# Kernel tuning notes

Hardware: AMD Instinct MI355X
Metric: run time of the kernel (lower is better)

## Reference

```python
import jax, jax.numpy as jnp
import numpy as np

D_MODEL = 1024


def pos_encoding(seq_len, d_model):
    # pos: [S,1], i: [d/2]
    pos = jnp.arange(seq_len, dtype=jnp.float32)[:, None]
    i = jnp.arange(0, d_model, 2, dtype=jnp.float32)
    angle_rates = 1.0 / jnp.power(10000.0, i / d_model)
    angle_rads = pos * angle_rates  # [S, d/2]
    # NOTE: original concatenates sin block then cos block (not interleaved)
    return jnp.concatenate([jnp.sin(angle_rads), jnp.cos(angle_rads)], axis=-1)  # [S, d]


def setup_inputs() -> dict:
    key = jax.random.key(0)
    ks = jax.random.split(key, 4)
    B, S, D = 4, 2048, D_MODEL
    scale = 1.0 / np.sqrt(D)
    x = jax.random.normal(ks[0], (B, S, D), dtype=jnp.float32)
    Wq = jax.random.normal(ks[1], (D, D), dtype=jnp.float32) * scale
    Wk = jax.random.normal(ks[2], (D, D), dtype=jnp.float32) * scale
    Wv = jax.random.normal(ks[3], (D, D), dtype=jnp.float32) * scale
    bq = jnp.zeros((D,), dtype=jnp.float32)
    bk = jnp.zeros((D,), dtype=jnp.float32)
    bv = jnp.zeros((D,), dtype=jnp.float32)
    return {"x": x, "Wq": Wq, "bq": bq, "Wk": Wk, "bk": bk, "Wv": Wv, "bv": bv}


def reference(x, Wq, bq, Wk, bk, Wv, bv):
    B, S, D = x.shape
    pe = pos_encoding(S, D)  # [S, D]
    h = x + pe[None, :, :]
    q = jnp.einsum('bsd,de->bse', h, Wq) + bq
    k = jnp.einsum('bsd,de->bse', h, Wk) + bk
    v = jnp.einsum('bsd,de->bse', h, Wv) + bv
    logits = jnp.einsum('bqd,bkd->bqk', q, k) / jnp.sqrt(jnp.float32(D))
    attn = jax.nn.softmax(logits, axis=-1)
    out = jnp.einsum('bqk,bkd->bqd', attn, v)
    return x + out
```

## Files before the change

kernel.cpp:

```cpp
#include <hip/hip_runtime.h>
#include <stdint.h>


#define AS1(p) ((__attribute__((address_space(1))) void*)(p))
#define AS3(p) ((__attribute__((address_space(3))) void*)(p))

typedef _Float16 f16x8 __attribute__((ext_vector_type(8)));
typedef _Float16 f16x4 __attribute__((ext_vector_type(4)));
typedef float f32x4 __attribute__((ext_vector_type(4)));

__global__ __launch_bounds__(256) void make_h(const float* __restrict__ x,
                                              _Float16* __restrict__ h) {
  const size_t gid = (size_t)blockIdx.x * 256 + threadIdx.x;
  const size_t e = gid * 4;
  const int d = (int)(e & 1023);
  const int m = (int)(e >> 10);
  const int s = m & 2047;
  const float4 xv = *(const float4*)(x + e);
  const int half = d >> 9;
  const int j0 = d & 511;
  const float c = -0.017988946039016f;
  float p[4];
#pragma unroll
  for (int t = 0; t < 4; t++) {
    const float r = __expf((float)(j0 + t) * c);
    const float a = (float)s * r;
    p[t] = half ? __cosf(a) : __sinf(a);
  }
  f16x4 o;
  o[0] = (_Float16)(xv.x + p[0]);
  o[1] = (_Float16)(xv.y + p[1]);
  o[2] = (_Float16)(xv.z + p[2]);
  o[3] = (_Float16)(xv.w + p[3]);
  *(f16x4*)(h + e) = o;
}

__global__ __launch_bounds__(256) void transpose_w(const float* __restrict__ Wq,
                                                   const float* __restrict__ Wk,
                                                   const float* __restrict__ Wv,
                                                   _Float16* __restrict__ Wt) {
  __shared__ float t[32][33];
  const int z = blockIdx.z;
  const float* W = (z == 0) ? Wq : (z == 1) ? Wk : Wv;
  _Float16* o = Wt + (size_t)z * 1024 * 1024;
  const int tx = threadIdx.x, ty = threadIdx.y;
  const int n0 = blockIdx.x * 32, k0 = blockIdx.y * 32;
#pragma unroll
  for (int i = ty; i < 32; i += 8)
    t[i][tx] = W[(size_t)(k0 + i) * 1024 + (n0 + tx)];
  __syncthreads();
#pragma unroll
  for (int i = ty; i < 32; i += 8)
    o[(size_t)(n0 + i) * 1024 + (k0 + tx)] = (_Float16)t[tx][i];
}

__global__ __launch_bounds__(256) void transpose_v(const _Float16* __restrict__ v,
                                                   _Float16* __restrict__ vT) {
  __shared__ _Float16 t[32][33];
  const int z = blockIdx.z;
  const _Float16* in = v + (size_t)z * 2048 * 1024;
  _Float16* out = vT + (size_t)z * 1024 * 2048;
  const int tx = threadIdx.x, ty = threadIdx.y;
  const int d0 = blockIdx.x * 32, j0 = blockIdx.y * 32;
#pragma unroll
  for (int i = ty; i < 32; i += 8)
    t[i][tx] = in[(size_t)(j0 + i) * 1024 + (d0 + tx)];
  __syncthreads();
#pragma unroll
  for (int i = ty; i < 32; i += 8)
    out[(size_t)(d0 + i) * 2048 + (j0 + tx)] = t[tx][i];
}

__global__ __launch_bounds__(256) void softmax_rows(const _Float16* __restrict__ L,
                                                    _Float16* __restrict__ P) {
  const size_t row = blockIdx.x;
  const _Float16* lr = L + row * 2048;
  _Float16* pr = P + row * 2048;
  const int tid = threadIdx.x;
  const f16x8 v = *(const f16x8*)(lr + tid * 8);
  float f[8];
#pragma unroll
  for (int t = 0; t < 8; t++) f[t] = (float)v[t];
  float mx = f[0];
#pragma unroll
  for (int t = 1; t < 8; t++) mx = fmaxf(mx, f[t]);
#pragma unroll
  for (int off = 32; off > 0; off >>= 1) mx = fmaxf(mx, __shfl_xor(mx, off));
  __shared__ float redm[4];
  __shared__ float reds[4];
  const int lane = tid & 63, wave = tid >> 6;
  if (lane == 0) redm[wave] = mx;
  __syncthreads();
  mx = fmaxf(fmaxf(redm[0], redm[1]), fmaxf(redm[2], redm[3]));
  float e[8];
  float sm = 0.f;
#pragma unroll
  for (int t = 0; t < 8; t++) { e[t] = __expf(f[t] - mx); sm += e[t]; }
#pragma unroll
  for (int off = 32; off > 0; off >>= 1) sm += __shfl_xor(sm, off);
  if (lane == 0) reds[wave] = sm;
  __syncthreads();
  sm = reds[0] + reds[1] + reds[2] + reds[3];
  const float inv = 1.0f / sm;
  f16x8 o;
#pragma unroll
  for (int t = 0; t < 8; t++) o[t] = (_Float16)(e[t] * inv);
  *(f16x8*)(pr + tid * 8) = o;
}

template <int MODE>
__global__ __launch_bounds__(256) void gemm_bt(
    const _Float16* __restrict__ A0, long long sA,
    const _Float16* __restrict__ B0, long long sB,
    void* __restrict__ C0, long long sC,
    const float* __restrict__ aux0, const float* __restrict__ aux1,
    const float* __restrict__ aux2, long long sX,
    const int K, const int N) {
  __shared__ __align__(16) _Float16 As[128 * 32];
  __shared__ __align__(16) _Float16 Bs[128 * 32];
  const int tid = threadIdx.x;
  const int z = blockIdx.z;
  const int bm0 = blockIdx.x * 128, bn0 = blockIdx.y * 128;
  const _Float16* A = A0 + (size_t)z * sA;
  const _Float16* Bt = B0 + (size_t)z * sB;

  const int srow = tid >> 2;
  const int csrc = (tid & 3) ^ ((tid >> 4) & 3);
  const _Float16* a0 = A + (size_t)(bm0 + srow) * K + csrc * 8;
  const _Float16* a1 = a0 + (size_t)64 * K;
  const _Float16* b0 = Bt + (size_t)(bn0 + srow) * K + csrc * 8;
  const _Float16* b1 = b0 + (size_t)64 * K;

  const int lane = tid & 63, wave = tid >> 6;
  const int wr = wave >> 1, wc = wave & 1;
  const int quad = lane >> 4, l16 = lane & 15;
  const int cq = (quad ^ ((l16 >> 2) & 3)) * 8;

  f32x4 acc[4][4];
#pragma unroll
  for (int i = 0; i < 4; i++)
#pragma unroll
    for (int j = 0; j < 4; j++) {
      f32x4 zz = {0.f, 0.f, 0.f, 0.f};
      acc[i][j] = zz;
    }

  for (int k0 = 0; k0 < K; k0 += 32) {
    __syncthreads();
    __builtin_amdgcn_global_load_lds(AS1(a0 + k0), AS3(&As[tid * 8]), 16, 0, 0);
    __builtin_amdgcn_global_load_lds(AS1(a1 + k0), AS3(&As[tid * 8 + 2048]), 16, 0, 0);
    __builtin_amdgcn_global_load_lds(AS1(b0 + k0), AS3(&Bs[tid * 8]), 16, 0, 0);
    __builtin_amdgcn_global_load_lds(AS1(b1 + k0), AS3(&Bs[tid * 8 + 2048]), 16, 0, 0);
    __syncthreads();
    f16x8 af[4], bfr[4];
#pragma unroll
    for (int i = 0; i < 4; i++)
      af[i] = *(const f16x8*)&As[(wr * 64 + i * 16 + l16) * 32 + cq];
#pragma unroll
    for (int j = 0; j < 4; j++)
      bfr[j] = *(const f16x8*)&Bs[(wc * 64 + j * 16 + l16) * 32 + cq];
#pragma unroll
    for (int i = 0; i < 4; i++)
#pragma unroll
      for (int j = 0; j < 4; j++)
        acc[i][j] = __builtin_amdgcn_mfma_f32_16x16x32_f16(af[i], bfr[j],
                                                           acc[i][j], 0, 0, 0);
  }

  const int rowb = bm0 + wr * 64 + quad * 4;
  const int colb = bn0 + wc * 64 + l16;
  if (MODE == 0 || MODE == 1) {
    _Float16* C = (_Float16*)C0 + (size_t)z * sC;
    const float* bias = (z == 0) ? aux0 : (z == 1) ? aux1 : aux2;
#pragma unroll
    for (int i = 0; i < 4; i++)
#pragma unroll
      for (int j = 0; j < 4; j++) {
        const int gn = colb + j * 16;
        const float bb = (MODE == 0) ? bias[gn] : 0.f;
#pragma unroll
        for (int r = 0; r < 4; r++) {
          const float val = (MODE == 0) ? (acc[i][j][r] + bb)
                                        : (acc[i][j][r] * 0.03125f);
          C[(size_t)(rowb + i * 16 + r) * N + gn] = (_Float16)val;
        }
      }
  } else {
    float* C = (float*)C0 + (size_t)z * sC;
    const float* X = aux0 + (size_t)z * sX;
#pragma unroll
    for (int i = 0; i < 4; i++)
#pragma unroll
      for (int j = 0; j < 4; j++)
#pragma unroll
        for (int r = 0; r < 4; r++) {
          const size_t idx = (size_t)(rowb + i * 16 + r) * N + (colb + j * 16);
          C[idx] = acc[i][j][r] + X[idx];
        }
  }
}

extern "C" void kernel_launch(void* const* d_in, const int* in_sizes, int n_in,
                              void* d_out, int out_size, void* d_ws, size_t ws_size,
                              hipStream_t stream) {
  (void)in_sizes; (void)n_in; (void)out_size; (void)ws_size;
  const float* x  = (const float*)d_in[0];
  const float* Wq = (const float*)d_in[1];
  const float* bq = (const float*)d_in[2];
  const float* Wk = (const float*)d_in[3];
  const float* bk = (const float*)d_in[4];
  const float* Wv = (const float*)d_in[5];
  const float* bv = (const float*)d_in[6];
  float* out = (float*)d_out;
  char* ws = (char*)d_ws;

  _Float16* h      = (_Float16*)(ws);
  _Float16* vT     = (_Float16*)(ws);
  _Float16* Wt     = (_Float16*)(ws + 16777216);
  _Float16* qkv    = (_Float16*)(ws + 23068672);
  _Float16* attn   = (_Float16*)(ws + 23068672);
  _Float16* logits = (_Float16*)(ws + 73400320);

  const long long E = 8388608;

  transpose_w<<<dim3(32, 32, 3), dim3(32, 8), 0, stream>>>(Wq, Wk, Wv, Wt);
  make_h<<<8192, 256, 0, stream>>>(x, h);

  gemm_bt<0><<<dim3(64, 8, 3), 256, 0, stream>>>(
      h, 0LL, Wt, 1048576LL, qkv, E, bq, bk, bv, 0LL, 1024, 1024);

  transpose_v<<<dim3(32, 64, 4), dim3(32, 8), 0, stream>>>(qkv + 2 * E, vT);

  gemm_bt<1><<<dim3(16, 16, 4), 256, 0, stream>>>(
      qkv, 2097152LL, qkv + E, 2097152LL, logits, 4194304LL,
      nullptr, nullptr, nullptr, 0LL, 1024, 2048);

  softmax_rows<<<8192, 256, 0, stream>>>(logits, attn);

  gemm_bt<2><<<dim3(16, 8, 4), 256, 0, stream>>>(
      attn, 4194304LL, vT, 2097152LL, out, 2097152LL,
      x, nullptr, nullptr, 2097152LL, 2048, 1024);
}
```

Before: 314.4 us.

## Fuse V transpose into QKV GEMM epilogue and write transposed vectorized outputs

The separate V transpose kernel is removed. The QKV projection now writes V directly in transposed layout from its epilogue. The logits and output GEMMs swap their A/B operand roles so each thread's accumulator column becomes contiguous, which allows 4-wide f16 and float4 stores and loads in the epilogues instead of scattered scalar accesses. This also drops the XOR swizzle on the LDS tile layout, which simplifies address math but risks LDS bank conflicts on the fragment reads.

```diff
diff --git a/kernel.cpp b/kernel.cpp
--- a/kernel.cpp
+++ b/kernel.cpp
@@ -54,23 +54,6 @@
     o[(size_t)(n0 + i) * 1024 + (k0 + tx)] = (_Float16)t[tx][i];
 }
 
-__global__ __launch_bounds__(256) void transpose_v(const _Float16* __restrict__ v,
-                                                   _Float16* __restrict__ vT) {
-  __shared__ _Float16 t[32][33];
-  const int z = blockIdx.z;
-  const _Float16* in = v + (size_t)z * 2048 * 1024;
-  _Float16* out = vT + (size_t)z * 1024 * 2048;
-  const int tx = threadIdx.x, ty = threadIdx.y;
-  const int d0 = blockIdx.x * 32, j0 = blockIdx.y * 32;
-#pragma unroll
-  for (int i = ty; i < 32; i += 8)
-    t[i][tx] = in[(size_t)(j0 + i) * 1024 + (d0 + tx)];
-  __syncthreads();
-#pragma unroll
-  for (int i = ty; i < 32; i += 8)
-    out[(size_t)(d0 + i) * 2048 + (j0 + tx)] = t[tx][i];
-}
-
 __global__ __launch_bounds__(256) void softmax_rows(const _Float16* __restrict__ L,
                                                     _Float16* __restrict__ P) {
   const size_t row = blockIdx.x;
@@ -112,10 +95,10 @@
 __global__ __launch_bounds__(256) void gemm_bt(
     const _Float16* __restrict__ A0, long long sA,
     const _Float16* __restrict__ B0, long long sB,
-    void* __restrict__ C0, long long sC,
+    void* __restrict__ C0, long long sC, void* __restrict__ C1,
     const float* __restrict__ aux0, const float* __restrict__ aux1,
     const float* __restrict__ aux2, long long sX,
-    const int K, const int N) {
+    const int K, const int N, const int ldc) {
   __shared__ __align__(16) _Float16 As[128 * 32];
   __shared__ __align__(16) _Float16 Bs[128 * 32];
   const int tid = threadIdx.x;
@@ -124,17 +107,14 @@
   const _Float16* A = A0 + (size_t)z * sA;
   const _Float16* Bt = B0 + (size_t)z * sB;
 
-  const int srow = tid >> 2;
-  const int csrc = (tid & 3) ^ ((tid >> 4) & 3);
-  const _Float16* a0 = A + (size_t)(bm0 + srow) * K + csrc * 8;
+  const _Float16* a0 = A + (size_t)(bm0 + (tid >> 2)) * K + (tid & 3) * 8;
   const _Float16* a1 = a0 + (size_t)64 * K;
-  const _Float16* b0 = Bt + (size_t)(bn0 + srow) * K + csrc * 8;
+  const _Float16* b0 = Bt + (size_t)(bn0 + (tid >> 2)) * K + (tid & 3) * 8;
   const _Float16* b1 = b0 + (size_t)64 * K;
 
   const int lane = tid & 63, wave = tid >> 6;
   const int wr = wave >> 1, wc = wave & 1;
   const int quad = lane >> 4, l16 = lane & 15;
-  const int cq = (quad ^ ((l16 >> 2) & 3)) * 8;
 
   f32x4 acc[4][4];
 #pragma unroll
@@ -155,10 +135,10 @@
     f16x8 af[4], bfr[4];
 #pragma unroll
     for (int i = 0; i < 4; i++)
-      af[i] = *(const f16x8*)&As[(wr * 64 + i * 16 + l16) * 32 + cq];
+      af[i] = *(const f16x8*)&As[(wr * 64 + i * 16 + l16) * 32 + quad * 8];
 #pragma unroll
     for (int j = 0; j < 4; j++)
-      bfr[j] = *(const f16x8*)&Bs[(wc * 64 + j * 16 + l16) * 32 + cq];
+      bfr[j] = *(const f16x8*)&Bs[(wc * 64 + j * 16 + l16) * 32 + quad * 8];
 #pragma unroll
     for (int i = 0; i < 4; i++)
 #pragma unroll
@@ -169,21 +149,47 @@
 
   const int rowb = bm0 + wr * 64 + quad * 4;
   const int colb = bn0 + wc * 64 + l16;
-  if (MODE == 0 || MODE == 1) {
+  if (MODE == 0) {
+    const float* bias = (z == 0) ? aux0 : (z == 1) ? aux1 : aux2;
+    if (z < 2) {
+      _Float16* C = (_Float16*)C0 + (size_t)z * sC;
+#pragma unroll
+      for (int i = 0; i < 4; i++)
+#pragma unroll
+        for (int j = 0; j < 4; j++) {
+          const int gn = colb + j * 16;
+          const float bb = bias[gn];
+#pragma unroll
+          for (int r = 0; r < 4; r++)
+            C[(size_t)(rowb + i * 16 + r) * N + gn] = (_Float16)(acc[i][j][r] + bb);
+        }
+    } else {
+      _Float16* VT = (_Float16*)C1;
+      const int b = rowb >> 11;
+      const int s0 = (rowb & 2047);
+#pragma unroll
+      for (int i = 0; i < 4; i++)
+#pragma unroll
+        for (int j = 0; j < 4; j++) {
+          const int gn = colb + j * 16;
+          const float bb = bias[gn];
+          f16x4 o;
+#pragma unroll
+          for (int r = 0; r < 4; r++) o[r] = (_Float16)(acc[i][j][r] + bb);
+          *(f16x4*)&VT[(size_t)b * 2097152 + (size_t)gn * 2048 + s0 + i * 16] = o;
+        }
+    }
+  } else if (MODE == 1) {
     _Float16* C = (_Float16*)C0 + (size_t)z * sC;
-    const float* bias = (z == 0) ? aux0 : (z == 1) ? aux1 : aux2;
 #pragma unroll
     for (int i = 0; i < 4; i++)
 #pragma unroll
       for (int j = 0; j < 4; j++) {
         const int gn = colb + j * 16;
-        const float bb = (MODE == 0) ? bias[gn] : 0.f;
-#pragma unroll
-        for (int r = 0; r < 4; r++) {
-          const float val = (MODE == 0) ? (acc[i][j][r] + bb)
-                                        : (acc[i][j][r] * 0.03125f);
-          C[(size_t)(rowb + i * 16 + r) * N + gn] = (_Float16)val;
-        }
+        f16x4 o;
+#pragma unroll
+        for (int r = 0; r < 4; r++) o[r] = (_Float16)(acc[i][j][r] * 0.03125f);
+        *(f16x4*)&C[(size_t)gn * ldc + rowb + i * 16] = o;
       }
   } else {
     float* C = (float*)C0 + (size_t)z * sC;
@@ -191,12 +197,17 @@
 #pragma unroll
     for (int i = 0; i < 4; i++)
 #pragma unroll
-      for (int j = 0; j < 4; j++)
-#pragma unroll
-        for (int r = 0; r < 4; r++) {
-          const size_t idx = (size_t)(rowb + i * 16 + r) * N + (colb + j * 16);
-          C[idx] = acc[i][j][r] + X[idx];
-        }
+      for (int j = 0; j < 4; j++) {
+        const int gn = colb + j * 16;
+        const size_t base = (size_t)gn * ldc + rowb + i * 16;
+        const float4 xv = *(const float4*)(X + base);
+        float4 o;
+        o.x = acc[i][j][0] + xv.x;
+        o.y = acc[i][j][1] + xv.y;
+        o.z = acc[i][j][2] + xv.z;
+        o.w = acc[i][j][3] + xv.w;
+        *(float4*)(C + base) = o;
+      }
   }
 }
 
@@ -215,10 +226,10 @@
   char* ws = (char*)d_ws;
 
   _Float16* h      = (_Float16*)(ws);
-  _Float16* vT     = (_Float16*)(ws);
   _Float16* Wt     = (_Float16*)(ws + 16777216);
-  _Float16* qkv    = (_Float16*)(ws + 23068672);
+  _Float16* qk     = (_Float16*)(ws + 23068672);
   _Float16* attn   = (_Float16*)(ws + 23068672);
+  _Float16* vT     = (_Float16*)(ws + 56623104);
   _Float16* logits = (_Float16*)(ws + 73400320);
 
   const long long E = 8388608;
@@ -227,17 +238,15 @@
   make_h<<<8192, 256, 0, stream>>>(x, h);
 
   gemm_bt<0><<<dim3(64, 8, 3), 256, 0, stream>>>(
-      h, 0LL, Wt, 1048576LL, qkv, E, bq, bk, bv, 0LL, 1024, 1024);
-
-  transpose_v<<<dim3(32, 64, 4), dim3(32, 8), 0, stream>>>(qkv + 2 * E, vT);
+      h, 0LL, Wt, 1048576LL, qk, E, vT, bq, bk, bv, 0LL, 1024, 1024, 0);
 
   gemm_bt<1><<<dim3(16, 16, 4), 256, 0, stream>>>(
-      qkv, 2097152LL, qkv + E, 2097152LL, logits, 4194304LL,
-      nullptr, nullptr, nullptr, 0LL, 1024, 2048);
+      qk + E, 2097152LL, qk, 2097152LL, logits, 4194304LL, nullptr,
+      nullptr, nullptr, nullptr, 0LL, 1024, 2048, 2048);
 
   softmax_rows<<<8192, 256, 0, stream>>>(logits, attn);
 
-  gemm_bt<2><<<dim3(16, 8, 4), 256, 0, stream>>>(
-      attn, 4194304LL, vT, 2097152LL, out, 2097152LL,
-      x, nullptr, nullptr, 2097152LL, 2048, 1024);
-}
+  gemm_bt<2><<<dim3(8, 16, 4), 256, 0, stream>>>(
+      vT, 2097152LL, attn, 4194304LL, out, 2097152LL, nullptr,
+      x, nullptr, nullptr, 2097152LL, 2048, 2048, 1024);
+}
```

Result: slower. 323.4 us (+2.8%).
